# Kernel optimization log

Hardware: AMD Instinct MI355X
Metric: run time of the kernel (lower is better)

## Reference

```python
import jax, jax.numpy as jnp
import numpy as np

CAP = 6.0
EPS = 1e-5

def _layernorm(x, g, b):
    mu = jnp.mean(x, axis=-1, keepdims=True)
    var = jnp.mean(jnp.square(x - mu), axis=-1, keepdims=True)
    return (x - mu) * jax.lax.rsqrt(var + EPS) * g + b

def setup_inputs() -> dict:
    key = jax.random.key(0)
    B, S, D, H = 4, 1024, 1024, 16
    DF = int(D * 2.0)
    ks = jax.random.split(key, 8)
    inp = {
        "x": jax.random.normal(ks[0], (B, S, D), dtype=jnp.float32),
        "mask": jnp.tril(jnp.ones((S, S), dtype=bool)),  # causal block mask
        "qkv_w": jax.random.normal(ks[1], (3 * D, D), dtype=jnp.float32) * 0.02,
        "qkv_b": jnp.zeros((3 * D,), dtype=jnp.float32),
        "out_w": jax.random.normal(ks[2], (D, D), dtype=jnp.float32) * 0.02,
        "out_b": jnp.zeros((D,), dtype=jnp.float32),
        "ln1_g": jnp.ones((D,), dtype=jnp.float32),
        "ln1_b": jnp.zeros((D,), dtype=jnp.float32),
        "ln2_g": jnp.ones((D,), dtype=jnp.float32),
        "ln2_b": jnp.zeros((D,), dtype=jnp.float32),
        "ff1_w": jax.random.normal(ks[3], (DF, D), dtype=jnp.float32) * 0.02,
        "ff1_b": jnp.zeros((DF,), dtype=jnp.float32),
        "ff2_w": jax.random.normal(ks[4], (D, DF), dtype=jnp.float32) * 0.02,
        "ff2_b": jnp.zeros((D,), dtype=jnp.float32),
    }
    return inp

def reference(x, mask, qkv_w, qkv_b, out_w, out_b, ln1_g, ln1_b, ln2_g, ln2_b,
              ff1_w, ff1_b, ff2_w, ff2_b):
    B, S, D = x.shape
    H = 16
    dh = D // H
    res = x
    h = _layernorm(x, ln1_g, ln1_b)
    qkv = h @ qkv_w.T + qkv_b                       # [B,S,3D]
    qkv = qkv.reshape(B, S, 3, H, dh).transpose(2, 0, 3, 1, 4)  # [3,B,H,S,dh]
    q, k, v = qkv[0], qkv[1], qkv[2]
    scores = jnp.einsum('bhqd,bhkd->bhqk', q, k) / jnp.sqrt(jnp.float32(dh))
    scores = CAP * jnp.tanh(scores / CAP)            # logit soft-cap score_mod
    scores = jnp.where(mask, scores, jnp.float32(-1e9))
    attn = jax.nn.softmax(scores, axis=-1)
    o = jnp.einsum('bhqk,bhkd->bhqd', attn, v)       # [B,H,S,dh]
    o = o.transpose(0, 2, 1, 3).reshape(B, S, D)
    x = res + (o @ out_w.T + out_b)
    h2 = _layernorm(x, ln2_g, ln2_b)
    ff = jax.nn.gelu(h2 @ ff1_w.T + ff1_b, approximate=False) @ ff2_w.T + ff2_b
    return x + ff
```

## Files before the change

### kernel.cpp

```cpp
#include <hip/hip_runtime.h>
#include <hip/hip_bf16.h>
#include <cmath>

#define NROWS 4096
#define DM    1024

typedef unsigned short u16;
typedef __attribute__((ext_vector_type(8))) short short8;
typedef __attribute__((ext_vector_type(4))) float floatx4;

#if __has_builtin(__builtin_amdgcn_exp2f)
#define EXP2F(x) __builtin_amdgcn_exp2f(x)
#else
#define EXP2F(x) exp2f(x)
#endif
#if __has_builtin(__builtin_amdgcn_rcpf)
#define RCPF(x) __builtin_amdgcn_rcpf(x)
#else
#define RCPF(x) (1.0f / (x))
#endif

__device__ __forceinline__ u16 f2bf(float f) {
    unsigned int u = __float_as_uint(f);
    return (u16)((u + 0x7fffu + ((u >> 16) & 1u)) >> 16);
}

__device__ __forceinline__ void gl_lds16(const u16* g, u16* l) {
    __builtin_amdgcn_global_load_lds(
        (const __attribute__((address_space(1))) unsigned int*)g,
        (__attribute__((address_space(3))) unsigned int*)l, 16, 0, 0);
}

__device__ __forceinline__ size_t pk_off(int row, int k, int KB) {
    const int rt = row >> 6, i = (row >> 4) & 3, lr = row & 15;
    const int kb = k >> 6, s = (k >> 5) & 1, lq = (k >> 3) & 3, j = k & 7;
    return ((((size_t)(rt * KB + kb) * 2 + s) * 4 + i) * 64 + lq * 16 + lr) * 8 + j;
}

__global__ __launch_bounds__(256) void castln_kernel(
    const float* __restrict__ s0, const float* __restrict__ s1,
    const float* __restrict__ s2, const float* __restrict__ s3,
    u16* __restrict__ d0, u16* __restrict__ d1,
    u16* __restrict__ d2, u16* __restrict__ d3,
    const float* __restrict__ x, const float* __restrict__ g,
    const float* __restrict__ beta, u16* __restrict__ hout)
{
    const int bid = blockIdx.x;
    if (bid < 8192) {
        const float* s; u16* d; int base, kbits, KB;
        if (bid < 3072)      { s = s0; d = d0; base = bid;        kbits = 10; KB = 16; }
        else if (bid < 4096) { s = s1; d = d1; base = bid - 3072; kbits = 10; KB = 16; }
        else if (bid < 6144) { s = s2; d = d2; base = bid - 4096; kbits = 10; KB = 16; }
        else                 { s = s3; d = d3; base = bid - 6144; kbits = 11; KB = 32; }
        const int idx = (base * 256 + threadIdx.x) * 4;
        const float4 v = *(const float4*)(s + idx);
        const int row = idx >> kbits, k = idx & ((1 << kbits) - 1);
        *(ushort4*)(d + pk_off(row, k, KB)) =
            make_ushort4(f2bf(v.x), f2bf(v.y), f2bf(v.z), f2bf(v.w));
        return;
    }
    const int row = bid - 8192;
    const int t = threadIdx.x;
    const float4 v = ((const float4*)(x + (size_t)row * DM))[t];
    float s = v.x + v.y + v.z + v.w;
    #pragma unroll
    for (int off = 32; off > 0; off >>= 1) s += __shfl_xor(s, off);
    __shared__ float red[4];
    const int wid = t >> 6;
    if ((t & 63) == 0) red[wid] = s;
    __syncthreads();
    const float mean = (red[0] + red[1] + red[2] + red[3]) * (1.0f / DM);
    const float dx = v.x - mean, dy = v.y - mean, dz = v.z - mean, dw = v.w - mean;
    float ss = dx*dx + dy*dy + dz*dz + dw*dw;
    #pragma unroll
    for (int off = 32; off > 0; off >>= 1) ss += __shfl_xor(ss, off);
    __syncthreads();
    if ((t & 63) == 0) red[wid] = ss;
    __syncthreads();
    const float var = (red[0] + red[1] + red[2] + red[3]) * (1.0f / DM);
    const float rstd = rsqrtf(var + 1e-5f);
    const float4 gv = ((const float4*)g)[t];
    const float4 bv = ((const float4*)beta)[t];
    *(ushort4*)(hout + pk_off(row, t * 4, 16)) = make_ushort4(
        f2bf(dx * rstd * gv.x + bv.x), f2bf(dy * rstd * gv.y + bv.y),
        f2bf(dz * rstd * gv.z + bv.z), f2bf(dw * rstd * gv.w + bv.w));
}

__global__ __launch_bounds__(256) void ln_kernel(
    const float* __restrict__ x, const float* __restrict__ g,
    const float* __restrict__ beta, u16* __restrict__ out)
{
    const int row = blockIdx.x;
    const int t = threadIdx.x;
    const float4 v = ((const float4*)(x + (size_t)row * DM))[t];
    float s = v.x + v.y + v.z + v.w;
    #pragma unroll
    for (int off = 32; off > 0; off >>= 1) s += __shfl_xor(s, off);
    __shared__ float red[4];
    const int wid = t >> 6;
    if ((t & 63) == 0) red[wid] = s;
    __syncthreads();
    const float mean = (red[0] + red[1] + red[2] + red[3]) * (1.0f / DM);
    const float dx = v.x - mean, dy = v.y - mean, dz = v.z - mean, dw = v.w - mean;
    float ss = dx*dx + dy*dy + dz*dz + dw*dw;
    #pragma unroll
    for (int off = 32; off > 0; off >>= 1) ss += __shfl_xor(ss, off);
    __syncthreads();
    if ((t & 63) == 0) red[wid] = ss;
    __syncthreads();
    const float var = (red[0] + red[1] + red[2] + red[3]) * (1.0f / DM);
    const float rstd = rsqrtf(var + 1e-5f);
    const float4 gv = ((const float4*)g)[t];
    const float4 bv = ((const float4*)beta)[t];
    *(ushort4*)(out + pk_off(row, t * 4, 16)) = make_ushort4(
        f2bf(dx * rstd * gv.x + bv.x), f2bf(dy * rstd * gv.y + bv.y),
        f2bf(dz * rstd * gv.z + bv.z), f2bf(dw * rstd * gv.w + bv.w));
}

__device__ __forceinline__ float gelu_f(float v) {
    return 0.5f * v * (1.0f + erff(v * 0.70710678118654752f));
}

template <int ACT, int OUTMODE, int TM>
__global__ __launch_bounds__(256, TM == 128 ? 3 : 4) void gemm_pk_kernel(
    const u16* __restrict__ A, const u16* __restrict__ W,
    const float* __restrict__ bias, const float* __restrict__ res,
    void* __restrict__ Cout, u16* __restrict__ vpout, u16* __restrict__ kpout,
    int N, int K)
{
    constexpr int MI = TM / 32;
    constexpr int NCH = (TM == 128) ? 4 : 3;
    constexpr int STAGEB = NCH * 8192;
    constexpr int EPIB = (OUTMODE == 1) ? 34816 : 17408;
    constexpr int SMEMB = (STAGEB > EPIB) ? STAGEB : EPIB;
    __shared__ __align__(16) char smem[SMEMB];
    u16* St = (u16*)smem;
    float* Cs = (float*)smem;

    const int tid = threadIdx.x;
    const int w = tid >> 6, l = tid & 63;
    const int lr = l & 15, lq = l >> 4;
    const int wm = w >> 1, wn = w & 1;

    const int fid = blockIdx.x;
    const int NB = (N >> 7) >> 3;
    const int xcd = fid & 7;
    const int kk = fid >> 3;
    constexpr int MT_BITS = (TM == 128) ? 5 : 6;
    constexpr int MT_MASK = (1 << MT_BITS) - 1;
    const int nt = xcd * NB + (kk >> MT_BITS);
    const int mt = kk & MT_MASK;
    const int m0 = mt * TM, n0 = nt * 128;
    const int KB = K >> 6;

    const u16* gch[NCH];
    if (TM == 128) {
        gch[0] = A + (size_t)(mt * 2 + 0) * KB * 4096;
        gch[1] = A + (size_t)(mt * 2 + 1) * KB * 4096;
        gch[2] = W + (size_t)(nt * 2 + 0) * KB * 4096;
        gch[3] = W + (size_t)(nt * 2 + 1) * KB * 4096;
    } else {
        gch[0] = A + (size_t)mt * KB * 4096;
        gch[1] = W + (size_t)(nt * 2 + 0) * KB * 4096;
        gch[2] = W + (size_t)(nt * 2 + 1) * KB * 4096;
    }

    floatx4 acc[MI][4] = {};

    auto STAGE = [&](int kb) {
        #pragma unroll
        for (int c = 0; c < NCH; c++) {
            const u16* src = gch[c] + (size_t)kb * 4096 + w * 512 + l * 8;
            u16* ld = St + c * 4096 + w * 512;
            gl_lds16(src, ld);
            gl_lds16(src + 2048, ld + 2048);
        }
    };

    auto COMPUTE = [&]() {
        #pragma unroll
        for (int ts = 0; ts < 2; ts++) {
            short8 af[MI], bf[4];
            #pragma unroll
            for (int i = 0; i < MI; i++) {
                const int off = (TM == 128) ? (wm * 4096 + ts * 2048 + i * 512)
                                            : (ts * 2048 + (wm * 2 + i) * 512);
                af[i] = *(const short8*)(St + off + l * 8);
            }
            constexpr int BB = (TM == 128) ? 2 : 1;
            #pragma unroll
            for (int j = 0; j < 4; j++)
                bf[j] = *(const short8*)(St + (BB + wn) * 4096 + ts * 2048 + j * 512 + l * 8);
            #pragma unroll
            for (int i = 0; i < MI; i++)
                #pragma unroll
                for (int j = 0; j < 4; j++)
                    acc[i][j] = __builtin_amdgcn_mfma_f32_16x16x32_bf16(af[i], bf[j], acc[i][j], 0, 0, 0);
        }
    };

    const int NKB = K >> 6;
    for (int kb = 0; kb < NKB; kb++) {
        STAGE(kb);
        __syncthreads();
        COMPUTE();
        __syncthreads();
    }

    if (OUTMODE == 1) {
        short* Ts = (short*)smem;
        float bj[4];
        #pragma unroll
        for (int j = 0; j < 4; j++) bj[j] = bias[n0 + wn * 64 + j * 16 + lr];
        const bool isV = (n0 >= 2048);
        if (isV) {
            #pragma unroll
            for (int i = 0; i < 4; i++)
                #pragma unroll
                for (int j = 0; j < 4; j++) {
                    const int vcol_l = wn * 64 + j * 16 + lr;
                    const int sbase = wm * 64 + i * 16 + lq * 4;
                    #pragma unroll
                    for (int rp = 0; rp < 2; rp++) {
                        const unsigned pkv =
                            (unsigned)f2bf(acc[i][j][rp * 2] + bj[j]) |
                            ((unsigned)f2bf(acc[i][j][rp * 2 + 1] + bj[j]) << 16);
                        *(unsigned*)&Ts[vcol_l * 136 + sbase + rp * 2] = pkv;
                    }
                }
        } else {
            #pragma unroll
            for (int i = 0; i < 4; i++)
                #pragma unroll
                for (int j = 0; j < 4; j++)
                    #pragma unroll
                    for (int r = 0; r < 4; r++) {
                        const int row_l = wm * 64 + i * 16 + lq * 4 + r;
                        const int col_l = wn * 64 + j * 16 + lr;
                        Ts[row_l * 136 + col_l] = (short)f2bf(acc[i][j][r] + bj[j]);
                    }
        }
        __syncthreads();
        u16* dbuf = isV ? vpout : (n0 >= 1024 ? kpout : (u16*)Cout);
        const int hbase = (n0 & 1023) >> 6;
        const int l0 = (tid * 2) & 63, subp = tid >> 6, sp = (tid >> 5) & 1;
        #pragma unroll
        for (int tl = 0; tl < 2; tl++) {
            const int mg = m0 + tl * 64;
            const int bb2 = mg >> 10, ktile = (mg & 1023) >> 6;
            #pragma unroll
            for (int hl = 0; hl < 2; hl++) {
                const int hh = hbase + hl;
                u16* dst = dbuf + ((size_t)(bb2 * 16 + hh) * 16 + ktile) * 4096 + tid * 16;
                #pragma unroll
                for (int half = 0; half < 2; half++) {
                    const int ll = l0 + half;
                    short8 seg;
                    if (isV) {
                        const int vcol_l = hl * 64 + subp * 16 + (ll & 15);
                        const int srow = tl * 64 + sp * 32 + ((ll >> 4) & 3) * 8;
                        seg = *(const short8*)&Ts[vcol_l * 136 + srow];
                    } else {
                        const int row_l = tl * 64 + subp * 16 + (ll & 15);
                        const int col_l = hl * 64 + sp * 32 + ((ll >> 4) & 3) * 8;
                        seg = *(const short8*)&Ts[row_l * 136 + col_l];
                    }
                    *(short8*)(dst + half * 8) = seg;
                }
            }
        }
        return;
    }

    #pragma unroll
    for (int i = 0; i < MI; i++) {
        __syncthreads();
        #pragma unroll
        for (int r = 0; r < 4; r++) {
            const int rl = wm * 16 + lq * 4 + r;
            #pragma unroll
            for (int j = 0; j < 4; j++)
                Cs[rl * 136 + wn * 64 + j * 16 + lr] = acc[i][j][r];
        }
        __syncthreads();
        #pragma unroll
        for (int q = 0; q < 2; q++) {
            const int s2 = tid * 2 + q;
            const int rid = s2 >> 4, c8 = s2 & 15;
            const int rr = m0 + (rid >> 4) * (TM / 2) + i * 16 + (rid & 15);
            const int col = c8 * 8;
            float vv[8];
            const float4 v0 = *(const float4*)&Cs[rid * 136 + col];
            const float4 v1 = *(const float4*)&Cs[rid * 136 + col + 4];
            const float4 ba = *(const float4*)&bias[n0 + col];
            const float4 bb4 = *(const float4*)&bias[n0 + col + 4];
            vv[0] = v0.x + ba.x;  vv[1] = v0.y + ba.y;  vv[2] = v0.z + ba.z;  vv[3] = v0.w + ba.w;
            vv[4] = v1.x + bb4.x; vv[5] = v1.y + bb4.y; vv[6] = v1.z + bb4.z; vv[7] = v1.w + bb4.w;
            if (ACT) {
                #pragma unroll
                for (int e = 0; e < 8; e++) vv[e] = gelu_f(vv[e]);
            }
            if (OUTMODE == 0) {
                const size_t o0 = (size_t)rr * N + n0 + col;
                if (res) {
                    const float4 r0 = *(const float4*)&res[o0];
                    const float4 r1 = *(const float4*)&res[o0 + 4];
                    vv[0]+=r0.x; vv[1]+=r0.y; vv[2]+=r0.z; vv[3]+=r0.w;
                    vv[4]+=r1.x; vv[5]+=r1.y; vv[6]+=r1.z; vv[7]+=r1.w;
                }
                *(float4*)((float*)Cout + o0)     = make_float4(vv[0], vv[1], vv[2], vv[3]);
                *(float4*)((float*)Cout + o0 + 4) = make_float4(vv[4], vv[5], vv[6], vv[7]);
            } else {
                short8 ov;
                #pragma unroll
                for (int e = 0; e < 8; e++) ov[e] = (short)f2bf(vv[e]);
                *(short8*)((u16*)Cout + pk_off(rr, n0 + col, N >> 6)) = ov;
            }
        }
    }
}

__global__ __launch_bounds__(256, 3) void attn_mfma_kernel(
    const u16* __restrict__ qp, const u16* __restrict__ kp,
    const u16* __restrict__ vp, u16* __restrict__ o)
{
    __shared__ __align__(16) short Ps[4][1152];
    __shared__ __align__(16) short Os[4096];
    __shared__ __align__(16) u16 Kl[2][4096];
    __shared__ __align__(16) u16 Vl[2][4096];

    const int qt = 15 - blockIdx.y;
    const int bh = blockIdx.x;
    const int b = bh >> 4, h = bh & 15;
    const int tid = threadIdx.x;
    const int w = tid >> 6, l = tid & 63;
    const int C = l & 15, Qd = l >> 4;

    const float C1f = 0.0601122935f, C2f = -17.3123404907f;

    const size_t headoff = (size_t)(b * 16 + h) * 16 * 4096;
    const u16* qb = qp + headoff + (size_t)qt * 4096 + w * 1024 + l * 8;
    const u16* kb = kp + headoff;
    const u16* vb = vp + headoff;

    short8 qf[2];
    qf[0] = *(const short8*)qb;
    qf[1] = *(const short8*)(qb + 512);

    float l_i = 0.f;
    floatx4 oacc[4] = {};

    auto STAGEKV = [&](int kt, int buf) {
        const u16* ks = kb + (size_t)kt * 4096 + (w * 2) * 512 + l * 8;
        const u16* vs = vb + (size_t)kt * 4096 + (w * 2) * 512 + l * 8;
        u16* kd = &Kl[buf][(w * 2) * 512];
        u16* vd = &Vl[buf][(w * 2) * 512];
        gl_lds16(ks, kd);
        gl_lds16(ks + 512, kd + 512);
        gl_lds16(vs, vd);
        gl_lds16(vs + 512, vd + 512);
    };

    int cur = 0;
    STAGEKV(0, 0);
    __syncthreads();

    for (int kt = 0; kt <= qt; kt++) {
        if (kt < qt) STAGEKV(kt + 1, cur ^ 1);

        const u16* Kc = &Kl[cur][0];
        const u16* Vc = &Vl[cur][0];
        short8 kf[8];
        #pragma unroll
        for (int i = 0; i < 8; i++) kf[i] = *(const short8*)(Kc + i * 512 + l * 8);

        floatx4 sacc[4] = {};
        #pragma unroll
        for (int mt = 0; mt < 4; mt++)
            #pragma unroll
            for (int s = 0; s < 2; s++)
                sacc[mt] = __builtin_amdgcn_mfma_f32_16x16x32_bf16(kf[mt * 2 + s], qf[s], sacc[mt], 0, 0, 0);

        float p[16];
        float rs = 0.f;
        const bool diag = (kt == qt);
        const int qrow = qt * 64 + w * 16 + C;
        #pragma unroll
        for (int mt = 0; mt < 4; mt++)
            #pragma unroll
            for (int r = 0; r < 4; r++) {
                const float e = EXP2F(sacc[mt][r] * C1f);
                float pv = EXP2F(C2f * RCPF(e + 1.0f));
                if (diag) {
                    const int krow = kt * 64 + mt * 16 + Qd * 4 + r;
                    if (krow > qrow) pv = 0.f;
                }
                p[mt * 4 + r] = pv;
                rs += pv;
            }
        rs += __shfl_xor(rs, 16);
        rs += __shfl_xor(rs, 32);
        l_i += rs;

        #pragma unroll
        for (int mt = 0; mt < 4; mt++)
            #pragma unroll
            for (int pr = 0; pr < 2; pr++) {
                union { __hip_bfloat162 b2; unsigned u; } cv;
                cv.b2 = __float22bfloat162_rn(
                    make_float2(p[mt * 4 + pr * 2], p[mt * 4 + pr * 2 + 1]));
                *(unsigned*)&Ps[w][C * 72 + mt * 16 + Qd * 4 + pr * 2] = cv.u;
            }
        short8 pf[2];
        pf[0] = *(const short8*)&Ps[w][C * 72 + Qd * 8];
        pf[1] = *(const short8*)&Ps[w][C * 72 + 32 + Qd * 8];

        short8 vf[8];
        #pragma unroll
        for (int j = 0; j < 8; j++) vf[j] = *(const short8*)(Vc + j * 512 + l * 8);

        #pragma unroll
        for (int dt = 0; dt < 4; dt++)
            #pragma unroll
            for (int s = 0; s < 2; s++)
                oacc[dt] = __builtin_amdgcn_mfma_f32_16x16x32_bf16(pf[s], vf[dt * 2 + s], oacc[dt], 0, 0, 0);

        __syncthreads();
        cur ^= 1;
    }

    float linv[4];
    #pragma unroll
    for (int r = 0; r < 4; r++) linv[r] = RCPF(__shfl(l_i, Qd * 4 + r));
    #pragma unroll
    for (int dt = 0; dt < 4; dt++) {
        const int s = dt >> 1;
        const int lqp = (dt & 1) * 2 + (C >> 3);
        const int jj = C & 7;
        #pragma unroll
        for (int r = 0; r < 4; r++)
            Os[((s * 4 + w) * 64 + lqp * 16 + Qd * 4 + r) * 8 + jj] =
                (short)f2bf(oacc[dt][r] * linv[r]);
    }
    __syncthreads();
    u16* obase = o + (size_t)((b * 16 + qt) * 16 + h) * 4096 + tid * 16;
    *(short8*)obase       = *(const short8*)&Os[tid * 16];
    *(short8*)(obase + 8) = *(const short8*)&Os[tid * 16 + 8];
}

extern "C" void kernel_launch(void* const* d_in, const int* in_sizes, int n_in,
                              void* d_out, int out_size, void* d_ws, size_t ws_size,
                              hipStream_t stream)
{
    (void)in_sizes; (void)n_in; (void)out_size; (void)ws_size;
    const float* x     = (const float*)d_in[0];
    const float* qkv_w = (const float*)d_in[2];
    const float* qkv_b = (const float*)d_in[3];
    const float* out_w = (const float*)d_in[4];
    const float* out_b = (const float*)d_in[5];
    const float* ln1_g = (const float*)d_in[6];
    const float* ln1_b = (const float*)d_in[7];
    const float* ln2_g = (const float*)d_in[8];
    const float* ln2_b = (const float*)d_in[9];
    const float* ff1_w = (const float*)d_in[10];
    const float* ff1_b = (const float*)d_in[11];
    const float* ff2_w = (const float*)d_in[12];
    const float* ff2_b = (const float*)d_in[13];
    float* out = (float*)d_out;

    u16* qpbuf = (u16*)d_ws;
    u16* kpbuf = qpbuf + 4194304;
    u16* vpbuf = kpbuf + 4194304;
    u16* hbuf  = (u16*)((char*)d_ws + 33554432);
    u16* obuf  = (u16*)((char*)d_ws + 41943040);
    u16* wq    = (u16*)((char*)d_ws + 50331648);
    u16* wo = wq + 3145728;
    u16* w1 = wo + 1048576;
    u16* w2 = w1 + 2097152;
    u16* ff1buf = (u16*)d_ws;

    castln_kernel<<<12288, 256, 0, stream>>>(
        qkv_w, out_w, ff1_w, ff2_w, wq, wo, w1, w2, x, ln1_g, ln1_b, hbuf);
    gemm_pk_kernel<0,1,128><<<768, 256, 0, stream>>>(
        hbuf, wq, qkv_b, nullptr, qpbuf, vpbuf, kpbuf, 3072, 1024);
    attn_mfma_kernel<<<dim3(64, 16), 256, 0, stream>>>(qpbuf, kpbuf, vpbuf, obuf);
    gemm_pk_kernel<0,0,64><<<512, 256, 0, stream>>>(
        obuf, wo, out_b, x, out, nullptr, nullptr, 1024, 1024);
    ln_kernel<<<NROWS, 256, 0, stream>>>(out, ln2_g, ln2_b, hbuf);
    gemm_pk_kernel<1,2,128><<<512, 256, 0, stream>>>(
        hbuf, w1, ff1_b, nullptr, ff1buf, nullptr, nullptr, 2048, 1024);
    gemm_pk_kernel<0,0,64><<<512, 256, 0, stream>>>(
        ff1buf, w2, ff2_b, out, out, nullptr, nullptr, 1024, 2048);
}
```

Measured before the change: 275.2 us.

## Double-buffer LDS staging in GEMM main loop to overlap loads with MFMA

Splits LDS into two buffers and prefetches the next k-phase while computing the current one, dropping one barrier per iteration. For the 128-row tile it halves each phase to a 32-wide k slice so the double buffer fits in the same LDS footprint. The aim is to hide global-to-LDS latency behind MFMA work. The cost is a larger LDS footprint for the 64-row variant, which may lower occupancy, and a doubled phase count for the 128 variant.

```diff
diff --git a/kernel.cpp b/kernel.cpp
--- a/kernel.cpp
+++ b/kernel.cpp
@@ -130,9 +130,10 @@
 {
     constexpr int MI = TM / 32;
     constexpr int NCH = (TM == 128) ? 4 : 3;
-    constexpr int STAGEB = NCH * 8192;
+    constexpr int PHE = (TM == 128) ? 8192 : 12288;
+    constexpr int DBUFB = 2 * PHE * 2;
     constexpr int EPIB = (OUTMODE == 1) ? 34816 : 17408;
-    constexpr int SMEMB = (STAGEB > EPIB) ? STAGEB : EPIB;
+    constexpr int SMEMB = (DBUFB > EPIB) ? DBUFB : EPIB;
     __shared__ __align__(16) char smem[SMEMB];
     u16* St = (u16*)smem;
     float* Cs = (float*)smem;
@@ -167,44 +168,67 @@
 
     floatx4 acc[MI][4] = {};
 
-    auto STAGE = [&](int kb) {
-        #pragma unroll
-        for (int c = 0; c < NCH; c++) {
-            const u16* src = gch[c] + (size_t)kb * 4096 + w * 512 + l * 8;
-            u16* ld = St + c * 4096 + w * 512;
-            gl_lds16(src, ld);
-            gl_lds16(src + 2048, ld + 2048);
+    auto STAGE = [&](int p, int buf) {
+        if (TM == 128) {
+            const int kb = p >> 1, s = p & 1;
+            #pragma unroll
+            for (int c = 0; c < NCH; c++)
+                gl_lds16(gch[c] + (size_t)kb * 4096 + s * 2048 + w * 512 + l * 8,
+                         St + buf * PHE + c * 2048 + w * 512);
+        } else {
+            #pragma unroll
+            for (int c = 0; c < NCH; c++) {
+                const u16* src = gch[c] + (size_t)p * 4096 + w * 512 + l * 8;
+                u16* dst = St + buf * PHE + c * 4096 + w * 512;
+                gl_lds16(src, dst);
+                gl_lds16(src + 2048, dst + 2048);
+            }
         }
     };
 
-    auto COMPUTE = [&]() {
-        #pragma unroll
-        for (int ts = 0; ts < 2; ts++) {
-            short8 af[MI], bf[4];
-            #pragma unroll
-            for (int i = 0; i < MI; i++) {
-                const int off = (TM == 128) ? (wm * 4096 + ts * 2048 + i * 512)
-                                            : (ts * 2048 + (wm * 2 + i) * 512);
-                af[i] = *(const short8*)(St + off + l * 8);
-            }
-            constexpr int BB = (TM == 128) ? 2 : 1;
+    auto COMPUTE = [&](int buf) {
+        const u16* Sb = St + buf * PHE;
+        if (TM == 128) {
+            short8 af[4], bf[4];
+            #pragma unroll
+            for (int i = 0; i < 4; i++)
+                af[i] = *(const short8*)(Sb + wm * 2048 + i * 512 + l * 8);
             #pragma unroll
             for (int j = 0; j < 4; j++)
-                bf[j] = *(const short8*)(St + (BB + wn) * 4096 + ts * 2048 + j * 512 + l * 8);
-            #pragma unroll
-            for (int i = 0; i < MI; i++)
+                bf[j] = *(const short8*)(Sb + (2 + wn) * 2048 + j * 512 + l * 8);
+            #pragma unroll
+            for (int i = 0; i < 4; i++)
                 #pragma unroll
                 for (int j = 0; j < 4; j++)
                     acc[i][j] = __builtin_amdgcn_mfma_f32_16x16x32_bf16(af[i], bf[j], acc[i][j], 0, 0, 0);
+        } else {
+            #pragma unroll
+            for (int ts = 0; ts < 2; ts++) {
+                short8 af[2], bf[4];
+                #pragma unroll
+                for (int i = 0; i < 2; i++)
+                    af[i] = *(const short8*)(Sb + ts * 2048 + (wm * 2 + i) * 512 + l * 8);
+                #pragma unroll
+                for (int j = 0; j < 4; j++)
+                    bf[j] = *(const short8*)(Sb + (1 + wn) * 4096 + ts * 2048 + j * 512 + l * 8);
+                #pragma unroll
+                for (int i = 0; i < 2; i++)
+                    #pragma unroll
+                    for (int j = 0; j < 4; j++)
+                        acc[i][j] = __builtin_amdgcn_mfma_f32_16x16x32_bf16(af[i], bf[j], acc[i][j], 0, 0, 0);
+            }
         }
     };
 
-    const int NKB = K >> 6;
-    for (int kb = 0; kb < NKB; kb++) {
-        STAGE(kb);
+    const int NPH = (TM == 128) ? (K >> 5) : (K >> 6);
+    STAGE(0, 0);
+    __syncthreads();
+    int cur = 0;
+    for (int p = 0; p < NPH; p++) {
+        if (p + 1 < NPH) STAGE(p + 1, cur ^ 1);
+        COMPUTE(cur);
         __syncthreads();
-        COMPUTE();
-        __syncthreads();
+        cur ^= 1;
     }
 
     if (OUTMODE == 1) {
```

Result: faster. 269.7 us (-2.0%).
